# Performance work log

Measured on AMD Instinct MI355X. Metric: run time of the kernel, lower is better.

The kernel has to match this reference:

```python
import jax, jax.numpy as jnp
from jax import lax
import numpy as np

B, T, H = 8192, 1024, 10


def setup_inputs() -> dict:
    key = jax.random.key(0)
    ks = jax.random.split(key, 7)
    s = 1.0 / np.sqrt(H)  # PyTorch default init scale for LSTM/Linear
    return {
        "x": jax.random.normal(ks[0], (B, T, 1), dtype=jnp.float32),
        "W_ih": jax.random.uniform(ks[1], (4 * H, 1), jnp.float32, -s, s),
        "W_hh": jax.random.uniform(ks[2], (4 * H, H), jnp.float32, -s, s),
        "b_ih": jax.random.uniform(ks[3], (4 * H,), jnp.float32, -s, s),
        "b_hh": jax.random.uniform(ks[4], (4 * H,), jnp.float32, -s, s),
        "W_lin": jax.random.uniform(ks[5], (1, H), jnp.float32, -s, s),
        "b_lin": jax.random.uniform(ks[6], (1,), jnp.float32, -s, s),
    }


def reference(x, W_ih, W_hh, b_ih, b_hh, W_lin, b_lin):
    # x: [B, T, 1] (batch_first). PyTorch gate order: i, f, g, o.
    b = b_ih + b_hh  # [4H]
    # Precompute input projections for all timesteps: [T, B, 4H]
    xg = jnp.einsum("bti,gi->tbg", x, W_ih) + b

    def step(carry, xg_t):
        h, c = carry  # each [B, H]
        gates = xg_t + h @ W_hh.T  # [B, 4H]
        i, f, g, o = jnp.split(gates, 4, axis=-1)
        c = jax.nn.sigmoid(f) * c + jax.nn.sigmoid(i) * jnp.tanh(g)
        h = jax.nn.sigmoid(o) * jnpp_tanh(c) if False else jax.nn.sigmoid(o) * jnp.tanh(c)
        return (h, c), None

    h0 = jnp.zeros((x.shape[0], W_hh.shape[1]), x.dtype)
    (_, cT), _ = lax.scan(step, (h0, h0), xg)
    # Module uses the final CELL state c_n, reshaped to [B, H], then Linear(10,1)
    return cT @ W_lin.T + b_lin  # [B, 1]
```

## Files before the change

### kernel.cpp

```cpp
#include <hip/hip_runtime.h>

#define B_TOT 8192
#define T_LEN 1024
#define HID 10

typedef float v2f __attribute__((ext_vector_type(2)));


#define BCAST16(v, K)                                                         \
    __int_as_float(__builtin_amdgcn_update_dpp(                               \
        __float_as_int(v), __float_as_int(v), 0x150 | (K), 0xF, 0xF, false))

__global__ __launch_bounds__(256) void lstm_fused_kernel(
    const float* __restrict__ x,
    const float* __restrict__ W_ih,
    const float* __restrict__ W_hh,
    const float* __restrict__ b_ih,
    const float* __restrict__ b_hh,
    const float* __restrict__ W_lin,
    const float* __restrict__ b_lin,
    float* __restrict__ out)
{
    const int tid  = threadIdx.x;
    const int j16  = tid & 15;
    const int b    = blockIdx.x * 16 + (tid >> 4);
    const bool act = (j16 < HID);
    const int j    = act ? j16 : 0;

    const float NL = -1.4426950408889634f;
    const float TL =  2.8853900817779268f;

    v2f w01[HID], w23[HID];
    v2f wi01, wi23, b01, b23;
    {
        const int r0 = 0 * HID + j, r1 = 1 * HID + j;
        const int r2 = 2 * HID + j, r3 = 3 * HID + j;
        wi01 = (v2f){NL * W_ih[r0], NL * W_ih[r1]};
        wi23 = (v2f){TL * W_ih[r2], NL * W_ih[r3]};
        b01  = (v2f){NL * (b_ih[r0] + b_hh[r0]), NL * (b_ih[r1] + b_hh[r1])};
        b23  = (v2f){TL * (b_ih[r2] + b_hh[r2]), NL * (b_ih[r3] + b_hh[r3])};
#pragma unroll
        for (int k = 0; k < HID; ++k) {
            w01[k] = (v2f){NL * W_hh[r0 * HID + k], NL * W_hh[r1 * HID + k]};
            w23[k] = (v2f){TL * W_hh[r2 * HID + k], NL * W_hh[r3 * HID + k]};
        }
    }
    const float wl = act ? W_lin[j] * 0.34657359027997264f : 0.0f;

    float h = 0.0f, C = 0.0f;
    const float* xb = x + (size_t)b * T_LEN;

#define ACC(K, A01, A23)                                                      \
    {                                                                         \
        float hk = BCAST16(h, K);                                             \
        v2f hk2 = (v2f){hk, hk};                                              \
        A01 = __builtin_elementwise_fma(w01[K], hk2, A01);                    \
        A23 = __builtin_elementwise_fma(w23[K], hk2, A23);                    \
    }

#define LSTM_STEP(xv)                                                         \
    {                                                                         \
        v2f xv2 = (v2f){(xv), (xv)};                                          \
        v2f a01 = __builtin_elementwise_fma(xv2, wi01, b01);                  \
        v2f a23 = __builtin_elementwise_fma(xv2, wi23, b23);                  \
        v2f s01 = (v2f){0.0f, 0.0f}, s23 = (v2f){0.0f, 0.0f};                 \
        ACC(0, a01, a23) ACC(1, a01, a23) ACC(2, a01, a23)                    \
        ACC(3, a01, a23) ACC(4, a01, a23)                                     \
        ACC(5, s01, s23) ACC(6, s01, s23) ACC(7, s01, s23)                    \
        ACC(8, s01, s23) ACC(9, s01, s23)                                     \
        a01 += s01;                                                           \
        a23 += s23;                                                           \
        float ig = __builtin_amdgcn_rcpf(1.0f + __builtin_amdgcn_exp2f(a01.x)); \
        float fg = __builtin_amdgcn_rcpf(1.0f + __builtin_amdgcn_exp2f(a01.y)); \
        float rg = __builtin_amdgcn_rcpf(1.0f + __builtin_amdgcn_exp2f(a23.x)); \
        float og = __builtin_amdgcn_rcpf(1.0f + __builtin_amdgcn_exp2f(a23.y)); \
        float gg = fmaf(-2.0f * TL, rg, TL);              \
        C = fmaf(fg, C, ig * gg);                                             \
        float tc = fmaf(-2.0f,                                                \
                        __builtin_amdgcn_rcpf(1.0f + __builtin_amdgcn_exp2f(C)), \
                        1.0f);                                                \
        h = og * tc;                                                          \
    }

    float4 xq = *reinterpret_cast<const float4*>(xb);
    int t = 0;
    for (; t < T_LEN - 4; t += 4) {
        float4 xn = *reinterpret_cast<const float4*>(xb + t + 4);
        LSTM_STEP(xq.x)
        LSTM_STEP(xq.y)
        LSTM_STEP(xq.z)
        LSTM_STEP(xq.w)
        xq = xn;
    }
    LSTM_STEP(xq.x)
    LSTM_STEP(xq.y)
    LSTM_STEP(xq.z)
    LSTM_STEP(xq.w)

#undef LSTM_STEP
#undef ACC

    float v = act ? C * wl : 0.0f;
#pragma unroll
    for (int s = 1; s < 16; s <<= 1) v += __shfl_xor(v, s, 16);
    if (j16 == 0) out[b] = v + b_lin[0];
}

extern "C" void kernel_launch(void* const* d_in, const int* in_sizes, int n_in,
                              void* d_out, int out_size, void* d_ws, size_t ws_size,
                              hipStream_t stream) {
    const float* x     = (const float*)d_in[0];
    const float* W_ih  = (const float*)d_in[1];
    const float* W_hh  = (const float*)d_in[2];
    const float* b_ih  = (const float*)d_in[3];
    const float* b_hh  = (const float*)d_in[4];
    const float* W_lin = (const float*)d_in[5];
    const float* b_lin = (const float*)d_in[6];
    float* out = (float*)d_out;

    dim3 grid(B_TOT / 16), block(256);
    hipLaunchKernelGGL(lstm_fused_kernel, grid, block, 0, stream,
                       x, W_ih, W_hh, b_ih, b_hh, W_lin, b_lin, out);
}
```

Before: 356.7 us.

## Pack six batch rows per wavefront with ds_bpermute hidden-state broadcast

The kernel now packs 6 batch elements of 10 lanes each into every 64-lane wavefront, where before it used 16-lane groups with 6 idle lanes each. The idle-lane fraction drops from 37.5% to about 6%. DPP row broadcasts no longer fit the 10-lane groups, so each step gathers the hidden state with ten ds_bpermute operations per lane. Those go through the LDS crossbar and add latency on the serial recurrence path. The final reduction moves to shared memory, and blocks shrink to one wavefront.

```diff
diff --git a/kernel.cpp b/kernel.cpp
--- a/kernel.cpp
+++ b/kernel.cpp
@@ -3,15 +3,11 @@
 #define B_TOT 8192
 #define T_LEN 1024
 #define HID 10
+#define BPW 6
 
 typedef float v2f __attribute__((ext_vector_type(2)));
 
-
-#define BCAST16(v, K)                                                         \
-    __int_as_float(__builtin_amdgcn_update_dpp(                               \
-        __float_as_int(v), __float_as_int(v), 0x150 | (K), 0xF, 0xF, false))
-
-__global__ __launch_bounds__(256) void lstm_fused_kernel(
+__global__ __launch_bounds__(64) void lstm_fused_kernel(
     const float* __restrict__ x,
     const float* __restrict__ W_ih,
     const float* __restrict__ W_hh,
@@ -21,11 +17,15 @@
     const float* __restrict__ b_lin,
     float* __restrict__ out)
 {
-    const int tid  = threadIdx.x;
-    const int j16  = tid & 15;
-    const int b    = blockIdx.x * 16 + (tid >> 4);
-    const bool act = (j16 < HID);
-    const int j    = act ? j16 : 0;
+    const int lane = threadIdx.x;
+    const int grp  = lane / HID;
+    const int j    = lane - grp * HID;
+    const int grpc = grp < BPW ? grp : BPW - 1;
+    const int b    = blockIdx.x * BPW + grpc;
+    const int bc   = b < B_TOT ? b : B_TOT - 1;
+    const bool act = (grp < BPW) && (b < B_TOT);
+
+    const int pbase = 4 * HID * grpc;
 
     const float NL = -1.4426950408889634f;
     const float TL =  2.8853900817779268f;
@@ -45,29 +45,34 @@
             w23[k] = (v2f){TL * W_hh[r2 * HID + k], NL * W_hh[r3 * HID + k]};
         }
     }
-    const float wl = act ? W_lin[j] * 0.34657359027997264f : 0.0f;
+    const float wl = W_lin[j] * 0.34657359027997264f;
 
     float h = 0.0f, C = 0.0f;
-    const float* xb = x + (size_t)b * T_LEN;
+    const float* xb = x + (size_t)bc * T_LEN;
 
-#define ACC(K, A01, A23)                                                      \
+#define BC(K) __int_as_float(__builtin_amdgcn_ds_bpermute(pbase + 4 * (K), hbits))
+
+#define ACC(K, HK, A01, A23)                                                  \
     {                                                                         \
-        float hk = BCAST16(h, K);                                             \
-        v2f hk2 = (v2f){hk, hk};                                              \
+        v2f hk2 = (v2f){(HK), (HK)};                                          \
         A01 = __builtin_elementwise_fma(w01[K], hk2, A01);                    \
         A23 = __builtin_elementwise_fma(w23[K], hk2, A23);                    \
     }
 
 #define LSTM_STEP(xv)                                                         \
     {                                                                         \
+        const int hbits = __float_as_int(h);                                  \
+        float hk0 = BC(0), hk1 = BC(1), hk2_ = BC(2), hk3 = BC(3);            \
+        float hk4 = BC(4), hk5 = BC(5), hk6 = BC(6), hk7 = BC(7);             \
+        float hk8 = BC(8), hk9 = BC(9);                                       \
         v2f xv2 = (v2f){(xv), (xv)};                                          \
         v2f a01 = __builtin_elementwise_fma(xv2, wi01, b01);                  \
         v2f a23 = __builtin_elementwise_fma(xv2, wi23, b23);                  \
         v2f s01 = (v2f){0.0f, 0.0f}, s23 = (v2f){0.0f, 0.0f};                 \
-        ACC(0, a01, a23) ACC(1, a01, a23) ACC(2, a01, a23)                    \
-        ACC(3, a01, a23) ACC(4, a01, a23)                                     \
-        ACC(5, s01, s23) ACC(6, s01, s23) ACC(7, s01, s23)                    \
-        ACC(8, s01, s23) ACC(9, s01, s23)                                     \
+        ACC(0, hk0, a01, a23) ACC(1, hk1, a01, a23) ACC(2, hk2_, a01, a23)    \
+        ACC(3, hk3, a01, a23) ACC(4, hk4, a01, a23)                           \
+        ACC(5, hk5, s01, s23) ACC(6, hk6, s01, s23) ACC(7, hk7, s01, s23)     \
+        ACC(8, hk8, s01, s23) ACC(9, hk9, s01, s23)                           \
         a01 += s01;                                                           \
         a23 += s23;                                                           \
         float ig = __builtin_amdgcn_rcpf(1.0f + __builtin_amdgcn_exp2f(a01.x)); \
@@ -99,11 +104,17 @@
 
 #undef LSTM_STEP
 #undef ACC
+#undef BC
 
-    float v = act ? C * wl : 0.0f;
+    __shared__ float red[64];
+    red[lane] = act ? C * wl : 0.0f;
+    __syncthreads();
+    if (act && j == 0) {
+        float s = b_lin[0];
 #pragma unroll
-    for (int s = 1; s < 16; s <<= 1) v += __shfl_xor(v, s, 16);
-    if (j16 == 0) out[b] = v + b_lin[0];
+        for (int u = 0; u < HID; ++u) s += red[grpc * HID + u];
+        out[b] = s;
+    }
 }
 
 extern "C" void kernel_launch(void* const* d_in, const int* in_sizes, int n_in,
@@ -118,7 +129,7 @@
     const float* b_lin = (const float*)d_in[6];
     float* out = (float*)d_out;
 
-    dim3 grid(B_TOT / 16), block(256);
+    dim3 grid((B_TOT + BPW - 1) / BPW), block(64);
     hipLaunchKernelGGL(lstm_fused_kernel, grid, block, 0, stream,
                        x, W_ih, W_hh, b_ih, b_hh, W_lin, b_lin, out);
 }
```

New measurement: 333.4 us. 6.5% less time.

## Repack LSTM gate dot products along k with packed FMA and merge reciprocals

Applied to the files above, without the earlier changes.

Weights are repacked so that each packed FMA covers two hidden-state elements of one gate, and the input term and bias are folded in as a sixth pair (x, 1). Inline-asm v_pk_mul/v_pk_fma are used, and a horizontal add finishes each gate. The gate math is also rewritten to share reciprocals: i*g and o*tanh(c) each use one rcp of a product of (1+exp) terms, with clamps at 80 to avoid overflow. The aim is fewer transcendental ops and fewer dependent instructions on the serial recurrence, at the cost of extra clamps and slightly different rounding.

```diff
diff --git a/kernel.cpp b/kernel.cpp
--- a/kernel.cpp
+++ b/kernel.cpp
@@ -6,6 +6,16 @@
 
 typedef float v2f __attribute__((ext_vector_type(2)));
 
+__device__ __forceinline__ v2f pk_mul(v2f a, v2f b) {
+    v2f d;
+    asm("v_pk_mul_f32 %0, %1, %2" : "=v"(d) : "v"(a), "v"(b));
+    return d;
+}
+__device__ __forceinline__ v2f pk_fma(v2f a, v2f b, v2f c) {
+    v2f d;
+    asm("v_pk_fma_f32 %0, %1, %2, %3" : "=v"(d) : "v"(a), "v"(b), "v"(c));
+    return d;
+}
 
 #define BCAST16(v, K)                                                         \
     __int_as_float(__builtin_amdgcn_update_dpp(                               \
@@ -30,56 +40,58 @@
     const float NL = -1.4426950408889634f;
     const float TL =  2.8853900817779268f;
 
-    v2f w01[HID], w23[HID];
-    v2f wi01, wi23, b01, b23;
-    {
-        const int r0 = 0 * HID + j, r1 = 1 * HID + j;
-        const int r2 = 2 * HID + j, r3 = 3 * HID + j;
-        wi01 = (v2f){NL * W_ih[r0], NL * W_ih[r1]};
-        wi23 = (v2f){TL * W_ih[r2], NL * W_ih[r3]};
-        b01  = (v2f){NL * (b_ih[r0] + b_hh[r0]), NL * (b_ih[r1] + b_hh[r1])};
-        b23  = (v2f){TL * (b_ih[r2] + b_hh[r2]), NL * (b_ih[r3] + b_hh[r3])};
+    v2f w[4][6];
 #pragma unroll
-        for (int k = 0; k < HID; ++k) {
-            w01[k] = (v2f){NL * W_hh[r0 * HID + k], NL * W_hh[r1 * HID + k]};
-            w23[k] = (v2f){TL * W_hh[r2 * HID + k], NL * W_hh[r3 * HID + k]};
-        }
+    for (int q = 0; q < 4; ++q) {
+        const float sc = (q == 2) ? TL : NL;
+        const int r = q * HID + j;
+#pragma unroll
+        for (int kp = 0; kp < 5; ++kp)
+            w[q][kp] = (v2f){sc * W_hh[r * HID + 2 * kp],
+                             sc * W_hh[r * HID + 2 * kp + 1]};
+        w[q][5] = (v2f){sc * W_ih[r], sc * (b_ih[r] + b_hh[r])};
     }
     const float wl = act ? W_lin[j] * 0.34657359027997264f : 0.0f;
 
     float h = 0.0f, C = 0.0f;
     const float* xb = x + (size_t)b * T_LEN;
 
-#define ACC(K, A01, A23)                                                      \
-    {                                                                         \
-        float hk = BCAST16(h, K);                                             \
-        v2f hk2 = (v2f){hk, hk};                                              \
-        A01 = __builtin_elementwise_fma(w01[K], hk2, A01);                    \
-        A23 = __builtin_elementwise_fma(w23[K], hk2, A23);                    \
-    }
-
 #define LSTM_STEP(xv)                                                         \
     {                                                                         \
-        v2f xv2 = (v2f){(xv), (xv)};                                          \
-        v2f a01 = __builtin_elementwise_fma(xv2, wi01, b01);                  \
-        v2f a23 = __builtin_elementwise_fma(xv2, wi23, b23);                  \
-        v2f s01 = (v2f){0.0f, 0.0f}, s23 = (v2f){0.0f, 0.0f};                 \
-        ACC(0, a01, a23) ACC(1, a01, a23) ACC(2, a01, a23)                    \
-        ACC(3, a01, a23) ACC(4, a01, a23)                                     \
-        ACC(5, s01, s23) ACC(6, s01, s23) ACC(7, s01, s23)                    \
-        ACC(8, s01, s23) ACC(9, s01, s23)                                     \
-        a01 += s01;                                                           \
-        a23 += s23;                                                           \
-        float ig = __builtin_amdgcn_rcpf(1.0f + __builtin_amdgcn_exp2f(a01.x)); \
-        float fg = __builtin_amdgcn_rcpf(1.0f + __builtin_amdgcn_exp2f(a01.y)); \
-        float rg = __builtin_amdgcn_rcpf(1.0f + __builtin_amdgcn_exp2f(a23.x)); \
-        float og = __builtin_amdgcn_rcpf(1.0f + __builtin_amdgcn_exp2f(a23.y)); \
-        float gg = fmaf(-2.0f * TL, rg, TL);              \
-        C = fmaf(fg, C, ig * gg);                                             \
-        float tc = fmaf(-2.0f,                                                \
-                        __builtin_amdgcn_rcpf(1.0f + __builtin_amdgcn_exp2f(C)), \
-                        1.0f);                                                \
-        h = og * tc;                                                          \
+        v2f hp0, hp1, hp2, hp3, hp4, hx;                                      \
+        hp0.x = BCAST16(h, 0); hp0.y = BCAST16(h, 1);                         \
+        hp1.x = BCAST16(h, 2); hp1.y = BCAST16(h, 3);                         \
+        hp2.x = BCAST16(h, 4); hp2.y = BCAST16(h, 5);                         \
+        hp3.x = BCAST16(h, 6); hp3.y = BCAST16(h, 7);                         \
+        hp4.x = BCAST16(h, 8); hp4.y = BCAST16(h, 9);                         \
+        hx.x  = (xv);          hx.y  = 1.0f;                                  \
+        v2f q0 = pk_mul(w[0][0], hp0), q1 = pk_mul(w[1][0], hp0);             \
+        v2f q2 = pk_mul(w[2][0], hp0), q3 = pk_mul(w[3][0], hp0);             \
+        q0 = pk_fma(w[0][1], hp1, q0); q1 = pk_fma(w[1][1], hp1, q1);         \
+        q2 = pk_fma(w[2][1], hp1, q2); q3 = pk_fma(w[3][1], hp1, q3);         \
+        q0 = pk_fma(w[0][2], hp2, q0); q1 = pk_fma(w[1][2], hp2, q1);         \
+        q2 = pk_fma(w[2][2], hp2, q2); q3 = pk_fma(w[3][2], hp2, q3);         \
+        q0 = pk_fma(w[0][3], hp3, q0); q1 = pk_fma(w[1][3], hp3, q1);         \
+        q2 = pk_fma(w[2][3], hp3, q2); q3 = pk_fma(w[3][3], hp3, q3);         \
+        q0 = pk_fma(w[0][4], hp4, q0); q1 = pk_fma(w[1][4], hp4, q1);         \
+        q2 = pk_fma(w[2][4], hp4, q2); q3 = pk_fma(w[3][4], hp4, q3);         \
+        q0 = pk_fma(w[0][5], hx, q0);  q1 = pk_fma(w[1][5], hx, q1);          \
+        q2 = pk_fma(w[2][5], hx, q2);  q3 = pk_fma(w[3][5], hx, q3);          \
+        float a0 = q0.x + q0.y;                    \
+        float a1 = q1.x + q1.y;                    \
+        float a2 = fminf(q2.x + q2.y, 80.0f);      \
+        float a3 = q3.x + q3.y;                    \
+        float ei = __builtin_amdgcn_exp2f(a0);                                \
+        float ef = __builtin_amdgcn_exp2f(a1);                                \
+        float eg = __builtin_amdgcn_exp2f(a2);                                \
+        float eo = __builtin_amdgcn_exp2f(a3);                                \
+        float fg = __builtin_amdgcn_rcpf(1.0f + ef);                          \
+        float rp = __builtin_amdgcn_rcpf((1.0f + ei) * (1.0f + eg));          \
+        float igg = (eg - 1.0f) * rp * TL;         \
+        C = fminf(fmaf(fg, C, igg), 80.0f);                                   \
+        float eC = __builtin_amdgcn_exp2f(C);                                 \
+        float rq = __builtin_amdgcn_rcpf((1.0f + eo) * (1.0f + eC));          \
+        h = (eC - 1.0f) * rq;                      \
     }
 
     float4 xq = *reinterpret_cast<const float4*>(xb);
@@ -96,9 +108,7 @@
     LSTM_STEP(xq.y)
     LSTM_STEP(xq.z)
     LSTM_STEP(xq.w)
-
 #undef LSTM_STEP
-#undef ACC
 
     float v = act ? C * wl : 0.0f;
 #pragma unroll
```

Result: no change. 360.3 us (+1.0%).

## Merge LSTM gate reciprocals into shared rcp and use scalar FMAs

Applied to the files above, without the earlier changes.

Replaces the packed v2f FMAs with scalar FMAs and hoists all ten DPP broadcasts to the top of each step. It also rewrites the gate maths so the five reciprocals per step become two: one rcp over the product of the i, f, g denominators and one over the o and tanh(c) denominators. The aim is to cut transcendental-unit work on the serial recurrence. The cost is more multiplies, plus overflow risk in the products, which is guarded only by clamping C at 80. In the scaled domain (C holds -2·log2(e)·c) that clamp bounds c from below at about -27.7, not from above. No guard covers the exp2 of the gate pre-activations.

```diff
diff --git a/kernel.cpp b/kernel.cpp
--- a/kernel.cpp
+++ b/kernel.cpp
@@ -3,9 +3,6 @@
 #define B_TOT 8192
 #define T_LEN 1024
 #define HID 10
-
-typedef float v2f __attribute__((ext_vector_type(2)));
-
 
 #define BCAST16(v, K)                                                         \
     __int_as_float(__builtin_amdgcn_update_dpp(                               \
@@ -30,19 +27,19 @@
     const float NL = -1.4426950408889634f;
     const float TL =  2.8853900817779268f;
 
-    v2f w01[HID], w23[HID];
-    v2f wi01, wi23, b01, b23;
+    float w0[HID], w1[HID], w2[HID], w3[HID];
+    float wi0, wi1, wi2, wi3, bb0, bb1, bb2, bb3;
     {
-        const int r0 = 0 * HID + j, r1 = 1 * HID + j;
-        const int r2 = 2 * HID + j, r3 = 3 * HID + j;
-        wi01 = (v2f){NL * W_ih[r0], NL * W_ih[r1]};
-        wi23 = (v2f){TL * W_ih[r2], NL * W_ih[r3]};
-        b01  = (v2f){NL * (b_ih[r0] + b_hh[r0]), NL * (b_ih[r1] + b_hh[r1])};
-        b23  = (v2f){TL * (b_ih[r2] + b_hh[r2]), NL * (b_ih[r3] + b_hh[r3])};
+        const int r0 = 0*HID+j, r1 = 1*HID+j, r2 = 2*HID+j, r3 = 3*HID+j;
+        wi0 = NL*W_ih[r0]; wi1 = NL*W_ih[r1]; wi2 = TL*W_ih[r2]; wi3 = NL*W_ih[r3];
+        bb0 = NL*(b_ih[r0]+b_hh[r0]); bb1 = NL*(b_ih[r1]+b_hh[r1]);
+        bb2 = TL*(b_ih[r2]+b_hh[r2]); bb3 = NL*(b_ih[r3]+b_hh[r3]);
 #pragma unroll
         for (int k = 0; k < HID; ++k) {
-            w01[k] = (v2f){NL * W_hh[r0 * HID + k], NL * W_hh[r1 * HID + k]};
-            w23[k] = (v2f){TL * W_hh[r2 * HID + k], NL * W_hh[r3 * HID + k]};
+            w0[k] = NL*W_hh[r0*HID+k];
+            w1[k] = NL*W_hh[r1*HID+k];
+            w2[k] = TL*W_hh[r2*HID+k];
+            w3[k] = NL*W_hh[r3*HID+k];
         }
     }
     const float wl = act ? W_lin[j] * 0.34657359027997264f : 0.0f;
@@ -50,36 +47,50 @@
     float h = 0.0f, C = 0.0f;
     const float* xb = x + (size_t)b * T_LEN;
 
-#define ACC(K, A01, A23)                                                      \
-    {                                                                         \
-        float hk = BCAST16(h, K);                                             \
-        v2f hk2 = (v2f){hk, hk};                                              \
-        A01 = __builtin_elementwise_fma(w01[K], hk2, A01);                    \
-        A23 = __builtin_elementwise_fma(w23[K], hk2, A23);                    \
-    }
-
 #define LSTM_STEP(xv)                                                         \
     {                                                                         \
-        v2f xv2 = (v2f){(xv), (xv)};                                          \
-        v2f a01 = __builtin_elementwise_fma(xv2, wi01, b01);                  \
-        v2f a23 = __builtin_elementwise_fma(xv2, wi23, b23);                  \
-        v2f s01 = (v2f){0.0f, 0.0f}, s23 = (v2f){0.0f, 0.0f};                 \
-        ACC(0, a01, a23) ACC(1, a01, a23) ACC(2, a01, a23)                    \
-        ACC(3, a01, a23) ACC(4, a01, a23)                                     \
-        ACC(5, s01, s23) ACC(6, s01, s23) ACC(7, s01, s23)                    \
-        ACC(8, s01, s23) ACC(9, s01, s23)                                     \
-        a01 += s01;                                                           \
-        a23 += s23;                                                           \
-        float ig = __builtin_amdgcn_rcpf(1.0f + __builtin_amdgcn_exp2f(a01.x)); \
-        float fg = __builtin_amdgcn_rcpf(1.0f + __builtin_amdgcn_exp2f(a01.y)); \
-        float rg = __builtin_amdgcn_rcpf(1.0f + __builtin_amdgcn_exp2f(a23.x)); \
-        float og = __builtin_amdgcn_rcpf(1.0f + __builtin_amdgcn_exp2f(a23.y)); \
-        float gg = fmaf(-2.0f * TL, rg, TL);              \
-        C = fmaf(fg, C, ig * gg);                                             \
-        float tc = fmaf(-2.0f,                                                \
-                        __builtin_amdgcn_rcpf(1.0f + __builtin_amdgcn_exp2f(C)), \
-                        1.0f);                                                \
-        h = og * tc;                                                          \
+        float h0 = BCAST16(h, 0), h1 = BCAST16(h, 1);                         \
+        float h2 = BCAST16(h, 2), h3 = BCAST16(h, 3);                         \
+        float h4 = BCAST16(h, 4), h5 = BCAST16(h, 5);                         \
+        float h6 = BCAST16(h, 6), h7 = BCAST16(h, 7);                         \
+        float h8 = BCAST16(h, 8), h9 = BCAST16(h, 9);                         \
+        float a0 = fmaf((xv), wi0, bb0);                                      \
+        float a1 = fmaf((xv), wi1, bb1);                                      \
+        float a2 = fmaf((xv), wi2, bb2);                                      \
+        float a3 = fmaf((xv), wi3, bb3);                                      \
+        a0 = fmaf(w0[0],h0,a0); a1 = fmaf(w1[0],h0,a1);                       \
+        a2 = fmaf(w2[0],h0,a2); a3 = fmaf(w3[0],h0,a3);                       \
+        a0 = fmaf(w0[1],h1,a0); a1 = fmaf(w1[1],h1,a1);                       \
+        a2 = fmaf(w2[1],h1,a2); a3 = fmaf(w3[1],h1,a3);                       \
+        a0 = fmaf(w0[2],h2,a0); a1 = fmaf(w1[2],h2,a1);                       \
+        a2 = fmaf(w2[2],h2,a2); a3 = fmaf(w3[2],h2,a3);                       \
+        a0 = fmaf(w0[3],h3,a0); a1 = fmaf(w1[3],h3,a1);                       \
+        a2 = fmaf(w2[3],h3,a2); a3 = fmaf(w3[3],h3,a3);                       \
+        a0 = fmaf(w0[4],h4,a0); a1 = fmaf(w1[4],h4,a1);                       \
+        a2 = fmaf(w2[4],h4,a2); a3 = fmaf(w3[4],h4,a3);                       \
+        float s0 = w0[5]*h5, s1 = w1[5]*h5, s2 = w2[5]*h5, s3 = w3[5]*h5;     \
+        s0 = fmaf(w0[6],h6,s0); s1 = fmaf(w1[6],h6,s1);                       \
+        s2 = fmaf(w2[6],h6,s2); s3 = fmaf(w3[6],h6,s3);                       \
+        s0 = fmaf(w0[7],h7,s0); s1 = fmaf(w1[7],h7,s1);                       \
+        s2 = fmaf(w2[7],h7,s2); s3 = fmaf(w3[7],h7,s3);                       \
+        s0 = fmaf(w0[8],h8,s0); s1 = fmaf(w1[8],h8,s1);                       \
+        s2 = fmaf(w2[8],h8,s2); s3 = fmaf(w3[8],h8,s3);                       \
+        s0 = fmaf(w0[9],h9,s0); s1 = fmaf(w1[9],h9,s1);                       \
+        s2 = fmaf(w2[9],h9,s2); s3 = fmaf(w3[9],h9,s3);                       \
+        a0 += s0; a1 += s1; a2 += s2; a3 += s3;                               \
+        float ei = __builtin_amdgcn_exp2f(a0);                                \
+        float ef = __builtin_amdgcn_exp2f(a1);                                \
+        float eg = __builtin_amdgcn_exp2f(a2);                                \
+        float eo = __builtin_amdgcn_exp2f(a3);                                \
+        float pf  = 1.0f + ef;                                                \
+        float P   = (1.0f + ei) * (1.0f + eg);                                \
+        float rp3 = __builtin_amdgcn_rcpf(P * pf);                            \
+        float fg  = P * rp3;                                      \
+        float igg = TL * (eg - 1.0f) * pf * rp3;       \
+        C = fminf(fmaf(fg, C, igg), 80.0f);                                   \
+        float eC = __builtin_amdgcn_exp2f(C);                                 \
+        float rq = __builtin_amdgcn_rcpf((1.0f + eo) * (1.0f + eC));          \
+        h = (eC - 1.0f) * rq;                             \
     }
 
     float4 xq = *reinterpret_cast<const float4*>(xb);
@@ -96,9 +107,7 @@
     LSTM_STEP(xq.y)
     LSTM_STEP(xq.z)
     LSTM_STEP(xq.w)
-
 #undef LSTM_STEP
-#undef ACC
 
     float v = act ? C * wl : 0.0f;
 #pragma unroll
```

Measured after the change: 366.4 us. 1.03x slower.
